# Performance work log

Measured on AMD Instinct MI355X. Metric: run time of the kernel, lower is better.

The kernel has to match this reference:

```python
import jax, jax.numpy as jnp
import numpy as np

NUM_HEADS = 8
HEAD_DIM = 16
NEG_SLOPE = 0.2


def setup_inputs() -> dict:
    key = jax.random.key(0)
    k1, k2, k3, k4, k5 = jax.random.split(key, 5)
    N, E, D_IN, D_OUT = 100000, 1600000, 128, 128
    x = jax.random.normal(k1, (N, D_IN), dtype=jnp.float32)
    edge_indices = jax.random.randint(k2, (2, E), 0, N, dtype=jnp.int64)
    W = jax.random.normal(k3, (D_OUT, D_IN), dtype=jnp.float32) * (1.0 / np.sqrt(D_IN))
    src_attn = jax.random.normal(k4, (1, NUM_HEADS, HEAD_DIM), dtype=jnp.float32) * (1.0 / np.sqrt(HEAD_DIM))
    dst_attn = jax.random.normal(k5, (1, NUM_HEADS, HEAD_DIM), dtype=jnp.float32) * (1.0 / np.sqrt(HEAD_DIM))
    return {"x": x, "edge_indices": edge_indices, "W": W, "src_attn": src_attn, "dst_attn": dst_attn}


def reference(x, edge_indices, W, src_attn, dst_attn):
    N = x.shape[0]
    # add self loops (i, i) for every node
    loops = jnp.arange(N, dtype=edge_indices.dtype)
    ei = jnp.concatenate([edge_indices, jnp.stack([loops, loops])], axis=1)  # [2, E+N]
    row, col = ei[0], ei[1]

    # linear projection + head split: [N, H, hd]
    h = (x @ W.T).reshape(N, NUM_HEADS, HEAD_DIM)

    # per-node attention logits, gathered per edge: [E', H]
    s = jnp.sum(h * src_attn, axis=-1)  # [N, H]
    d = jnp.sum(h * dst_attn, axis=-1)  # [N, H]
    e = jax.nn.leaky_relu(s[row] + d[col], negative_slope=NEG_SLOPE)  # [E', H]

    # sparse softmax over each row's neighborhood (dim=1 of the sparse matrix)
    m = jax.ops.segment_max(e, row, num_segments=N)  # [N, H]
    e = jnp.exp(e - m[row])
    z = jax.ops.segment_sum(e, row, num_segments=N)  # [N, H]
    a = e / z[row]  # [E', H]

    # per-head SpMM: out[row] += a * h[col]
    out = jax.ops.segment_sum(a[:, :, None] * h[col], row, num_segments=N)  # [N, H, hd]
    return out.reshape(N, NUM_HEADS * HEAD_DIM)
```

## Files before the change

kernel.cpp:

```cpp
#include <hip/hip_runtime.h>
#include <hip/hip_bf16.h>
#include <math.h>

#define NEG_SLOPE 0.2f

typedef __attribute__((ext_vector_type(8))) short short8v;
typedef __attribute__((ext_vector_type(4))) float f32x4;

__global__ __launch_bounds__(256) void gat_prep(
    const float* __restrict__ W, const float* __restrict__ srcA,
    const float* __restrict__ dstA, ushort* __restrict__ wbf,
    int* __restrict__ count, int N,
    unsigned int* __restrict__ state, int* __restrict__ ticket)
{
  int gtid = blockIdx.x * 256 + threadIdx.x;
  for (int i = gtid; i < N; i += gridDim.x * 256)
    count[i] = 0;
  if (gtid < 256) state[gtid] = 0;
  if (gtid == 0) *ticket = 0;

  if (gtid >= 36 * 64) return;
  int frag = gtid >> 6, lane = gtid & 63;
  int nt = frag >> 2, ks = frag & 3;
  int kbase = ks * 32 + (lane >> 4) * 8;
  ushort v[8];
  if (nt < 8) {
    int r = nt * 16 + (lane & 15);
#pragma unroll
    for (int j = 0; j < 8; ++j)
      v[j] = __bfloat16_as_ushort(__float2bfloat16(W[(size_t)r * 128 + kbase + j]));
  } else {
    int n = lane & 15;
    int hd = n & 7;
    const float* av = (n < 8) ? srcA : dstA;
#pragma unroll
    for (int j = 0; j < 8; ++j) {
      float acc = 0.f;
      int k = kbase + j;
      for (int d = 0; d < 16; ++d)
        acc += W[(size_t)(hd * 16 + d) * 128 + k] * av[hd * 16 + d];
      v[j] = __bfloat16_as_ushort(__float2bfloat16(acc));
    }
  }
  ushort* dst = wbf + ((size_t)frag * 64 + lane) * 8;
#pragma unroll
  for (int j = 0; j < 8; ++j) dst[j] = v[j];
}

__global__ __launch_bounds__(256, 2) void gat_gemm_hist(
    const float* __restrict__ x, const ushort* __restrict__ wbf,
    ushort* __restrict__ hb, float* __restrict__ s, float* __restrict__ dv,
    int N, int nchunks, int G1,
    const int* __restrict__ ei, int E, int* __restrict__ count,
    int* __restrict__ rank, int userank)
{
  const int q = (int)blockIdx.x / 5;
  const int r5 = (int)blockIdx.x % 5;
  if (r5 == 0) {
    const int wave = threadIdx.x >> 6, lane = threadIdx.x & 63;
    const int lrow = lane & 15, lkg = lane >> 4;

    short8v b[36];
    const short8v* wv = (const short8v*)wbf;
#pragma unroll
    for (int f = 0; f < 36; ++f) b[f] = wv[(size_t)f * 64 + lane];

    for (int chunk = q; chunk < nchunks; chunk += G1) {
      const int r0 = chunk * 64 + wave * 16;
      int arow = r0 + lrow; if (arow > N - 1) arow = N - 1;
      const float* xr = x + (size_t)arow * 128 + lkg * 8;

      f32x4 acc[9];
#pragma unroll
      for (int t = 0; t < 9; ++t) acc[t] = (f32x4){0.f, 0.f, 0.f, 0.f};

#pragma unroll
      for (int ks = 0; ks < 4; ++ks) {
        float4 x0 = *(const float4*)(xr + ks * 32);
        float4 x1 = *(const float4*)(xr + ks * 32 + 4);
        short8v a;
        a[0] = (short)__bfloat16_as_ushort(__float2bfloat16(x0.x));
        a[1] = (short)__bfloat16_as_ushort(__float2bfloat16(x0.y));
        a[2] = (short)__bfloat16_as_ushort(__float2bfloat16(x0.z));
        a[3] = (short)__bfloat16_as_ushort(__float2bfloat16(x0.w));
        a[4] = (short)__bfloat16_as_ushort(__float2bfloat16(x1.x));
        a[5] = (short)__bfloat16_as_ushort(__float2bfloat16(x1.y));
        a[6] = (short)__bfloat16_as_ushort(__float2bfloat16(x1.z));
        a[7] = (short)__bfloat16_as_ushort(__float2bfloat16(x1.w));
#pragma unroll
        for (int t = 0; t < 9; ++t)
          acc[t] = __builtin_amdgcn_mfma_f32_16x16x32_bf16(a, b[t * 4 + ks], acc[t], 0, 0, 0);
      }

      const int rbase = r0 + lkg * 4;
#pragma unroll
      for (int t = 0; t < 8; ++t) {
#pragma unroll
        for (int r = 0; r < 4; ++r) {
          int row = rbase + r;
          if (row < N)
            hb[(size_t)row * 128 + t * 16 + lrow] =
                __bfloat16_as_ushort(__float2bfloat16(acc[t][r]));
        }
      }
#pragma unroll
      for (int r = 0; r < 4; ++r) {
        int row = rbase + r;
        if (row < N) {
          if (lrow < 8) s[(size_t)row * 8 + lrow] = acc[8][r];
          else          dv[(size_t)row * 8 + (lrow - 8)] = acc[8][r];
        }
      }
    }
  } else {
    __shared__ int sh64;
    if (threadIdx.x == 0) sh64 = 1;
    __syncthreads();
    if (ei[2 * threadIdx.x + 1] != 0) sh64 = 0;
    __syncthreads();
    const int is64 = sh64;

    const int hb_id = q * 4 + (r5 - 1);
    const int nhb = 4 * G1;
    int i = hb_id * 256 + threadIdx.x;
    const int stride = nhb * 256;
    for (; i < E; i += stride) {
      int r = is64 ? ei[2 * i] : ei[i];
      int old = atomicAdd(&count[r], 1);
      if (userank) rank[i] = old;
    }
  }
}

__global__ __launch_bounds__(256) void gat_scan(
    const int* __restrict__ count, int N, int nb,
    unsigned int* __restrict__ state, int* __restrict__ ticket,
    int* __restrict__ offsets, int* __restrict__ cursor, int total)
{
  __shared__ int sbid;
  __shared__ int sm[256];
  __shared__ int sprefix;
  if (threadIdx.x == 0) sbid = atomicAdd(ticket, 1);
  __syncthreads();
  const int bid = sbid;
  const int base = bid * 1024 + threadIdx.x * 4;

  int v0 = 0, v1 = 0, v2 = 0, v3 = 0;
  if (base + 0 < N) v0 = count[base + 0] + 1;
  if (base + 1 < N) v1 = count[base + 1] + 1;
  if (base + 2 < N) v2 = count[base + 2] + 1;
  if (base + 3 < N) v3 = count[base + 3] + 1;
  int tsum = v0 + v1 + v2 + v3;

  sm[threadIdx.x] = tsum;
  __syncthreads();
  int acc = tsum;
  for (int off = 1; off < 256; off <<= 1) {
    int other = (threadIdx.x >= off) ? sm[threadIdx.x - off] : 0;
    __syncthreads();
    acc += other;
    sm[threadIdx.x] = acc;
    __syncthreads();
  }
  const int blocktotal = sm[255];

  if (threadIdx.x == 0) {
    __hip_atomic_store(&state[bid], (1u << 30) | (unsigned)blocktotal,
                       __ATOMIC_RELEASE, __HIP_MEMORY_SCOPE_AGENT);
    int ex = 0;
    int j = bid - 1;
    while (j >= 0) {
      unsigned d = __hip_atomic_load(&state[j], __ATOMIC_ACQUIRE, __HIP_MEMORY_SCOPE_AGENT);
      unsigned st = d >> 30;
      if (st == 0u) continue;
      ex += (int)(d & 0x3FFFFFFFu);
      if (st >= 2u) break;
      --j;
    }
    __hip_atomic_store(&state[bid], (2u << 30) | (unsigned)(ex + blocktotal),
                       __ATOMIC_RELEASE, __HIP_MEMORY_SCOPE_AGENT);
    sprefix = ex;
  }
  __syncthreads();

  int e = sprefix + acc - tsum;
  if (base + 0 < N) { offsets[base + 0] = e; cursor[base + 0] = e; e += v0; }
  if (base + 1 < N) { offsets[base + 1] = e; cursor[base + 1] = e; e += v1; }
  if (base + 2 < N) { offsets[base + 2] = e; cursor[base + 2] = e; e += v2; }
  if (base + 3 < N) { offsets[base + 3] = e; cursor[base + 3] = e; e += v3; }
  if (bid == nb - 1 && threadIdx.x == 255) offsets[N] = total;
}

__global__ __launch_bounds__(256) void gat_scatter_rank(
    const int* __restrict__ ei, int E, int N,
    const int* __restrict__ offsets, const int* __restrict__ count,
    const int* __restrict__ rank, int* __restrict__ scol)
{
  __shared__ int sh64;
  if (threadIdx.x == 0) sh64 = 1;
  __syncthreads();
  if (ei[2 * threadIdx.x + 1] != 0) sh64 = 0;
  __syncthreads();
  const int is64 = sh64;

  int i = blockIdx.x * 256 + threadIdx.x;
  const int stride = gridDim.x * 256;
  const int total = E + N;
  for (; i < total; i += stride) {
    int pos, c;
    if (i < E) {
      int r;
      if (is64) { r = ei[2 * i]; c = ei[2 * (E + i)]; }
      else      { r = ei[i];     c = ei[E + i]; }
      pos = offsets[r] + rank[i];
    } else {
      int r = i - E; c = r;
      pos = offsets[r] + count[r];
    }
    scol[pos] = c;
  }
}

__global__ __launch_bounds__(256) void gat_scatter(
    const int* __restrict__ ei, int E, int N,
    int* __restrict__ cursor, int* __restrict__ scol)
{
  __shared__ int sh64;
  if (threadIdx.x == 0) sh64 = 1;
  __syncthreads();
  if (ei[2 * threadIdx.x + 1] != 0) sh64 = 0;
  __syncthreads();
  const int is64 = sh64;

  int i = blockIdx.x * 256 + threadIdx.x;
  const int stride = gridDim.x * 256;
  const int total = E + N;
  for (; i < total; i += stride) {
    int r, c;
    if (i < E) {
      if (is64) { r = ei[2 * i]; c = ei[2 * (E + i)]; }
      else      { r = ei[i];     c = ei[E + i]; }
    } else {
      r = i - E; c = r;
    }
    int pos = atomicAdd(&cursor[r], 1);
    scol[pos] = c;
  }
}

__global__ __launch_bounds__(256) void gat_agg(
    const uint* __restrict__ hb, const float* __restrict__ s, const float* __restrict__ dv,
    const int* __restrict__ offsets, const int* __restrict__ scol,
    float* __restrict__ out, int rowbase, int rowlim)
{
  int wid = rowbase + (int)((blockIdx.x * 256 + threadIdx.x) >> 6);
  int lane = threadIdx.x & 63;
  if (wid >= rowlim) return;
  const int g = lane >> 4;
  const int t = lane & 15;
  const int head = t >> 1;
  const int beg = __builtin_amdgcn_readfirstlane(offsets[wid]);
  const int end = __builtin_amdgcn_readfirstlane(offsets[wid + 1]);
  const float sl = s[wid * 8 + head];

  const char* hbp = (const char*)hb;
  const char* dvp = (const char*)dv;
  const uint hoff = (uint)t * 16u;
  const uint doff = (uint)head * 4u;

  float z = 0.f;
  float a0 = 0, a1 = 0, a2 = 0, a3 = 0, a4 = 0, a5 = 0, a6 = 0, a7 = 0;

  const int nq = (end - beg + 3) >> 2;
  const int lasti = end - 1;

  int iA = beg + g;       iA = iA < end ? iA : lasti;
  int iB = beg + 4 + g;   iB = iB < end ? iB : lasti;
  int iC = beg + 8 + g;   iC = iC < end ? iC : lasti;
  int cB = scol[iB];
  int cC = scol[iC];
  int cA = scol[iA];
  float dlA = *(const float*)(dvp + ((uint)cA * 32u + doff));
  uint4 huA = *(const uint4*)(hbp + ((uint)cA * 256u + hoff));
  float dlB = *(const float*)(dvp + ((uint)cB * 32u + doff));
  uint4 huB = *(const uint4*)(hbp + ((uint)cB * 256u + hoff));

  for (int j = 0; j < nq; ++j) {
    int iD = beg + 4 * (j + 3) + g; iD = iD < end ? iD : lasti;
    int cD = scol[iD];
    float dlC = *(const float*)(dvp + ((uint)cC * 32u + doff));
    uint4 huC = *(const uint4*)(hbp + ((uint)cC * 256u + hoff));

    float e = sl + dlA;
    e = fmaxf(e, NEG_SLOPE * e);
    float w = (beg + 4 * j + g < end) ? __expf(e) : 0.f;
    z += w;
    a0 = fmaf(w, __uint_as_float(huA.x << 16), a0);
    a1 = fmaf(w, __uint_as_float(huA.x & 0xFFFF0000u), a1);
    a2 = fmaf(w, __uint_as_float(huA.y << 16), a2);
    a3 = fmaf(w, __uint_as_float(huA.y & 0xFFFF0000u), a3);
    a4 = fmaf(w, __uint_as_float(huA.z << 16), a4);
    a5 = fmaf(w, __uint_as_float(huA.z & 0xFFFF0000u), a5);
    a6 = fmaf(w, __uint_as_float(huA.w << 16), a6);
    a7 = fmaf(w, __uint_as_float(huA.w & 0xFFFF0000u), a7);

    dlA = dlB; huA = huB;
    dlB = dlC; huB = huC;
    cC = cD;
  }

  a0 += __shfl_xor(a0, 16, 64); a0 += __shfl_xor(a0, 32, 64);
  a1 += __shfl_xor(a1, 16, 64); a1 += __shfl_xor(a1, 32, 64);
  a2 += __shfl_xor(a2, 16, 64); a2 += __shfl_xor(a2, 32, 64);
  a3 += __shfl_xor(a3, 16, 64); a3 += __shfl_xor(a3, 32, 64);
  a4 += __shfl_xor(a4, 16, 64); a4 += __shfl_xor(a4, 32, 64);
  a5 += __shfl_xor(a5, 16, 64); a5 += __shfl_xor(a5, 32, 64);
  a6 += __shfl_xor(a6, 16, 64); a6 += __shfl_xor(a6, 32, 64);
  a7 += __shfl_xor(a7, 16, 64); a7 += __shfl_xor(a7, 32, 64);
  z  += __shfl_xor(z, 16, 64);  z  += __shfl_xor(z, 32, 64);

  float inv = 1.f / z;
  if (lane < 16) {
    float4* op = (float4*)(out + (size_t)wid * 128 + t * 8);
    op[0] = make_float4(a0 * inv, a1 * inv, a2 * inv, a3 * inv);
    op[1] = make_float4(a4 * inv, a5 * inv, a6 * inv, a7 * inv);
  }
}

extern "C" void kernel_launch(void* const* d_in, const int* in_sizes, int n_in,
                              void* d_out, int out_size, void* d_ws, size_t ws_size,
                              hipStream_t stream) {
  const float* x    = (const float*)d_in[0];
  const int*   ei   = (const int*)d_in[1];
  const float* W    = (const float*)d_in[2];
  const float* srcA = (const float*)d_in[3];
  const float* dstA = (const float*)d_in[4];
  float* out = (float*)d_out;
  const int N = in_sizes[0] / 128;
  const int E = in_sizes[1] / 2;

  ushort* hbuf = (ushort*)d_ws;
  float* s  = (float*)(hbuf + (size_t)N * 128);
  float* dv = s + (size_t)N * 8;
  ushort* wbf = (ushort*)(dv + (size_t)N * 8);
  int* count   = (int*)((char*)wbf + 36864);
  int* offsets = count + N;
  int* cursor  = offsets + (N + 1);
  unsigned int* state = (unsigned int*)(cursor + N);
  int* ticket  = (int*)(state + 256);
  int* scol    = ticket + 4;
  int* rank    = scol + (E + N);

  const size_t need_rank = (size_t)((char*)(rank + E) - (char*)d_ws);
  const int userank = (ws_size >= need_rank) ? 1 : 0;

  const int nchunks = (N + 63) / 64;
  const int G1 = 512;

  gat_prep<<<2048, 256, 0, stream>>>(W, srcA, dstA, wbf, count, N, state, ticket);
  gat_gemm_hist<<<5 * G1, 256, 0, stream>>>(x, wbf, hbuf, s, dv, N, nchunks, G1,
                                            ei, E, count, rank, userank);
  const int nb = (N + 1023) / 1024;
  gat_scan<<<nb, 256, 0, stream>>>(count, N, nb, state, ticket, offsets, cursor, E + N);
  if (userank)
    gat_scatter_rank<<<2048, 256, 0, stream>>>(ei, E, N, offsets, count, rank, scol);
  else
    gat_scatter<<<2048, 256, 0, stream>>>(ei, E, N, cursor, scol);
  const int half = N / 2;
  gat_agg<<<(half + 3) / 4, 256, 0, stream>>>((const uint*)hbuf, s, dv, offsets, scol, out, 0, half);
  gat_agg<<<(N - half + 3) / 4, 256, 0, stream>>>((const uint*)hbuf, s, dv, offsets, scol, out, half, N);
}
```

Baseline: 225.3 us.

## Privatize degree histogram into 8 copies, warp-parallel scan lookback, single agg launch

The degree-count atomics are spread over 8 private histogram copies chosen by block index, which reduces contention on hot counters. Each edge's rank now encodes which copy it used. The scan sums the copies and writes per-copy sub-offsets plus a self-loop position, and the decoupled lookback now checks 64 predecessor states at once using wave ballots instead of walking them one by one. The two half-size aggregation launches are merged into one. The cost is 8x the counter memory plus an extra sub-offset array to zero, read and write. In the non-rank fallback path, selfpos is used as the atomic cursor.

Result: faster. 207.8 us (-7.7%).

```diff
diff --git a/kernel.cpp b/kernel.cpp
--- a/kernel.cpp
+++ b/kernel.cpp
@@ -10,12 +10,12 @@
 __global__ __launch_bounds__(256) void gat_prep(
     const float* __restrict__ W, const float* __restrict__ srcA,
     const float* __restrict__ dstA, ushort* __restrict__ wbf,
-    int* __restrict__ count, int N,
+    int* __restrict__ count8, int cn,
     unsigned int* __restrict__ state, int* __restrict__ ticket)
 {
   int gtid = blockIdx.x * 256 + threadIdx.x;
-  for (int i = gtid; i < N; i += gridDim.x * 256)
-    count[i] = 0;
+  for (int i = gtid; i < cn; i += gridDim.x * 256)
+    count8[i] = 0;
   if (gtid < 256) state[gtid] = 0;
   if (gtid == 0) *ticket = 0;
 
@@ -51,8 +51,8 @@
     const float* __restrict__ x, const ushort* __restrict__ wbf,
     ushort* __restrict__ hb, float* __restrict__ s, float* __restrict__ dv,
     int N, int nchunks, int G1,
-    const int* __restrict__ ei, int E, int* __restrict__ count,
-    int* __restrict__ rank, int userank)
+    const int* __restrict__ ei, int E, int* __restrict__ count8,
+    int* __restrict__ rank, int userank, int npriv)
 {
   const int q = (int)blockIdx.x / 5;
   const int r5 = (int)blockIdx.x % 5;
@@ -119,6 +119,8 @@
     if (ei[2 * threadIdx.x + 1] != 0) sh64 = 0;
     __syncthreads();
     const int is64 = sh64;
+    const int k = (int)(blockIdx.x & (unsigned)(npriv - 1));
+    int* cnt = count8 + (size_t)k * N;
 
     const int hb_id = q * 4 + (r5 - 1);
     const int nhb = 4 * G1;
@@ -126,16 +128,18 @@
     const int stride = nhb * 256;
     for (; i < E; i += stride) {
       int r = is64 ? ei[2 * i] : ei[i];
-      int old = atomicAdd(&count[r], 1);
-      if (userank) rank[i] = old;
-    }
-  }
-}
-
+      int old = atomicAdd(&cnt[r], 1);
+      if (userank) rank[i] = old | (k << 28);
+    }
+  }
+}
+
+template<int NPRIV>
 __global__ __launch_bounds__(256) void gat_scan(
-    const int* __restrict__ count, int N, int nb,
+    const int* __restrict__ count8, int N, int nb,
     unsigned int* __restrict__ state, int* __restrict__ ticket,
-    int* __restrict__ offsets, int* __restrict__ cursor, int total)
+    int* __restrict__ offsets, int* __restrict__ suboff,
+    int* __restrict__ selfpos, int total, int userank)
 {
   __shared__ int sbid;
   __shared__ int sm[256];
@@ -145,12 +149,21 @@
   const int bid = sbid;
   const int base = bid * 1024 + threadIdx.x * 4;
 
-  int v0 = 0, v1 = 0, v2 = 0, v3 = 0;
-  if (base + 0 < N) v0 = count[base + 0] + 1;
-  if (base + 1 < N) v1 = count[base + 1] + 1;
-  if (base + 2 < N) v2 = count[base + 2] + 1;
-  if (base + 3 < N) v3 = count[base + 3] + 1;
-  int tsum = v0 + v1 + v2 + v3;
+  int c[4][NPRIV];
+  int v[4];
+  int tsum = 0;
+#pragma unroll
+  for (int j = 0; j < 4; ++j) {
+    int idx = base + j;
+    int cs = 0;
+#pragma unroll
+    for (int k = 0; k < NPRIV; ++k) {
+      int cv = (idx < N) ? count8[(size_t)k * N + idx] : 0;
+      c[j][k] = cv; cs += cv;
+    }
+    v[j] = (idx < N) ? cs + 1 : 0;
+    tsum += v[j];
+  }
 
   sm[threadIdx.x] = tsum;
   __syncthreads();
@@ -164,36 +177,58 @@
   }
   const int blocktotal = sm[255];
 
-  if (threadIdx.x == 0) {
+  if (threadIdx.x == 0)
     __hip_atomic_store(&state[bid], (1u << 30) | (unsigned)blocktotal,
                        __ATOMIC_RELEASE, __HIP_MEMORY_SCOPE_AGENT);
+  if (threadIdx.x < 64) {
+    const int lane = threadIdx.x;
     int ex = 0;
     int j = bid - 1;
     while (j >= 0) {
-      unsigned d = __hip_atomic_load(&state[j], __ATOMIC_ACQUIRE, __HIP_MEMORY_SCOPE_AGENT);
+      int idx = j - lane;
+      unsigned d = (idx >= 0)
+          ? __hip_atomic_load(&state[idx], __ATOMIC_ACQUIRE, __HIP_MEMORY_SCOPE_AGENT)
+          : (2u << 30);
       unsigned st = d >> 30;
-      if (st == 0u) continue;
-      ex += (int)(d & 0x3FFFFFFFu);
-      if (st >= 2u) break;
-      --j;
-    }
-    __hip_atomic_store(&state[bid], (2u << 30) | (unsigned)(ex + blocktotal),
-                       __ATOMIC_RELEASE, __HIP_MEMORY_SCOPE_AGENT);
-    sprefix = ex;
+      unsigned long long m2 = __ballot(st == 2u);
+      unsigned long long m0 = __ballot(st == 0u);
+      int f2 = m2 ? ((int)__ffsll((long long)m2) - 1) : 64;
+      int f0 = m0 ? ((int)__ffsll((long long)m0) - 1) : 64;
+      if (f0 < f2) continue;
+      int take = (lane < f2 || (lane == f2 && f2 < 64)) ? (int)(d & 0x3FFFFFFFu) : 0;
+#pragma unroll
+      for (int off = 1; off < 64; off <<= 1) take += __shfl_xor(take, off, 64);
+      ex += take;
+      if (f2 < 64) break;
+      j -= 64;
+    }
+    if (lane == 0) {
+      __hip_atomic_store(&state[bid], (2u << 30) | (unsigned)(ex + blocktotal),
+                         __ATOMIC_RELEASE, __HIP_MEMORY_SCOPE_AGENT);
+      sprefix = ex;
+    }
   }
   __syncthreads();
 
   int e = sprefix + acc - tsum;
-  if (base + 0 < N) { offsets[base + 0] = e; cursor[base + 0] = e; e += v0; }
-  if (base + 1 < N) { offsets[base + 1] = e; cursor[base + 1] = e; e += v1; }
-  if (base + 2 < N) { offsets[base + 2] = e; cursor[base + 2] = e; e += v2; }
-  if (base + 3 < N) { offsets[base + 3] = e; cursor[base + 3] = e; e += v3; }
+#pragma unroll
+  for (int j = 0; j < 4; ++j) {
+    int idx = base + j;
+    if (idx < N) {
+      offsets[idx] = e;
+      int run = e;
+#pragma unroll
+      for (int k = 0; k < NPRIV; ++k) { suboff[(size_t)k * N + idx] = run; run += c[j][k]; }
+      selfpos[idx] = userank ? run : e;
+      e += v[j];
+    }
+  }
   if (bid == nb - 1 && threadIdx.x == 255) offsets[N] = total;
 }
 
 __global__ __launch_bounds__(256) void gat_scatter_rank(
     const int* __restrict__ ei, int E, int N,
-    const int* __restrict__ offsets, const int* __restrict__ count,
+    const int* __restrict__ suboff, const int* __restrict__ selfpos,
     const int* __restrict__ rank, int* __restrict__ scol)
 {
   __shared__ int sh64;
@@ -212,10 +247,12 @@
       int r;
       if (is64) { r = ei[2 * i]; c = ei[2 * (E + i)]; }
       else      { r = ei[i];     c = ei[E + i]; }
-      pos = offsets[r] + rank[i];
+      int pr = rank[i];
+      int k = (int)(((unsigned)pr) >> 28);
+      pos = suboff[(size_t)k * N + r] + (pr & 0x0FFFFFFF);
     } else {
       int r = i - E; c = r;
-      pos = offsets[r] + count[r];
+      pos = selfpos[r];
     }
     scol[pos] = c;
   }
@@ -251,11 +288,11 @@
 __global__ __launch_bounds__(256) void gat_agg(
     const uint* __restrict__ hb, const float* __restrict__ s, const float* __restrict__ dv,
     const int* __restrict__ offsets, const int* __restrict__ scol,
-    float* __restrict__ out, int rowbase, int rowlim)
-{
-  int wid = rowbase + (int)((blockIdx.x * 256 + threadIdx.x) >> 6);
+    float* __restrict__ out, int N)
+{
+  int wid = (int)((blockIdx.x * 256 + threadIdx.x) >> 6);
   int lane = threadIdx.x & 63;
-  if (wid >= rowlim) return;
+  if (wid >= N) return;
   const int g = lane >> 4;
   const int t = lane & 15;
   const int head = t >> 1;
@@ -339,34 +376,52 @@
   const int N = in_sizes[0] / 128;
   const int E = in_sizes[1] / 2;
 
+  auto need = [&](int npriv, int userank) -> size_t {
+    size_t b = (size_t)N * 128 * 2;
+    b += (size_t)N * 8 * 4 * 2;
+    b += 36864;
+    b += (size_t)npriv * N * 4;
+    b += (size_t)(N + 1) * 4;
+    b += (size_t)npriv * N * 4;
+    b += (size_t)N * 4;
+    b += 256 * 4 + 16;
+    b += (size_t)(E + N) * 4;
+    if (userank) b += (size_t)E * 4;
+    return b;
+  };
+  int npriv = 8, userank = 1;
+  if (need(8, 1) > ws_size) { npriv = 1; userank = 1; }
+  if (need(1, 1) > ws_size) { npriv = 1; userank = 0; }
+
   ushort* hbuf = (ushort*)d_ws;
   float* s  = (float*)(hbuf + (size_t)N * 128);
   float* dv = s + (size_t)N * 8;
   ushort* wbf = (ushort*)(dv + (size_t)N * 8);
-  int* count   = (int*)((char*)wbf + 36864);
-  int* offsets = count + N;
-  int* cursor  = offsets + (N + 1);
-  unsigned int* state = (unsigned int*)(cursor + N);
+  int* count8  = (int*)((char*)wbf + 36864);
+  int* offsets = count8 + (size_t)npriv * N;
+  int* suboff  = offsets + (N + 1);
+  int* selfpos = suboff + (size_t)npriv * N;
+  unsigned int* state = (unsigned int*)(selfpos + N);
   int* ticket  = (int*)(state + 256);
   int* scol    = ticket + 4;
   int* rank    = scol + (E + N);
 
-  const size_t need_rank = (size_t)((char*)(rank + E) - (char*)d_ws);
-  const int userank = (ws_size >= need_rank) ? 1 : 0;
-
   const int nchunks = (N + 63) / 64;
   const int G1 = 512;
-
-  gat_prep<<<2048, 256, 0, stream>>>(W, srcA, dstA, wbf, count, N, state, ticket);
+  const int nb = (N + 1023) / 1024;
+
+  gat_prep<<<2048, 256, 0, stream>>>(W, srcA, dstA, wbf, count8, npriv * N, state, ticket);
   gat_gemm_hist<<<5 * G1, 256, 0, stream>>>(x, wbf, hbuf, s, dv, N, nchunks, G1,
-                                            ei, E, count, rank, userank);
-  const int nb = (N + 1023) / 1024;
-  gat_scan<<<nb, 256, 0, stream>>>(count, N, nb, state, ticket, offsets, cursor, E + N);
+                                            ei, E, count8, rank, userank, npriv);
+  if (npriv == 8)
+    gat_scan<8><<<nb, 256, 0, stream>>>(count8, N, nb, state, ticket, offsets,
+                                        suboff, selfpos, E + N, userank);
+  else
+    gat_scan<1><<<nb, 256, 0, stream>>>(count8, N, nb, state, ticket, offsets,
+                                        suboff, selfpos, E + N, userank);
   if (userank)
-    gat_scatter_rank<<<2048, 256, 0, stream>>>(ei, E, N, offsets, count, rank, scol);
+    gat_scatter_rank<<<2048, 256, 0, stream>>>(ei, E, N, suboff, selfpos, rank, scol);
   else
-    gat_scatter<<<2048, 256, 0, stream>>>(ei, E, N, cursor, scol);
-  const int half = N / 2;
-  gat_agg<<<(half + 3) / 4, 256, 0, stream>>>((const uint*)hbuf, s, dv, offsets, scol, out, 0, half);
-  gat_agg<<<(N - half + 3) / 4, 256, 0, stream>>>((const uint*)hbuf, s, dv, offsets, scol, out, half, N);
-}
+    gat_scatter<<<2048, 256, 0, stream>>>(ei, E, N, selfpos, scol);
+  gat_agg<<<(N + 3) / 4, 256, 0, stream>>>((const uint*)hbuf, s, dv, offsets, scol, out, N);
+}
```
